# Kernel optimization log

Hardware: AMD Instinct MI355X
Metric: run time of the kernel (lower is better)

The kernel has to match this reference:

```python
import jax, jax.numpy as jnp
import numpy as np

N_NODES = 100000
N_EDGES = 1600000
N_LABEL = 200000
HID = 128
OUT = 5


def setup_inputs() -> dict:
    key = jax.random.key(0)
    k1, k2, k3, k4, k5 = jax.random.split(key, 5)
    x = jax.random.normal(k1, (N_NODES, HID), dtype=jnp.float32)
    edge_index = jax.random.randint(k2, (2, N_EDGES), 0, N_NODES, dtype=jnp.int64)
    edge_label_index = jax.random.randint(k3, (2, N_LABEL), 0, N_NODES, dtype=jnp.int64)
    W_gcn = jax.random.normal(k4, (HID, HID), dtype=jnp.float32) / np.sqrt(HID)
    b_gcn = jnp.zeros((HID,), dtype=jnp.float32)
    W_lin = jax.random.normal(k5, (2 * HID, OUT), dtype=jnp.float32) / np.sqrt(2 * HID)
    b_lin = jnp.zeros((OUT,), dtype=jnp.float32)
    return {"x": x, "edge_index": edge_index, "edge_label_index": edge_label_index,
            "W_gcn": W_gcn, "b_gcn": b_gcn, "W_lin": W_lin, "b_lin": b_lin}


def _gcn_conv(x, edge_index, W, b):
    # PyG GCNConv defaults: add self-loops, symmetric normalization,
    # linear transform first, then scatter-add of norm * x[src] into dst.
    n = x.shape[0]
    loop = jnp.arange(n, dtype=edge_index.dtype)
    src = jnp.concatenate([edge_index[0], loop])  # [E+N]
    dst = jnp.concatenate([edge_index[1], loop])  # [E+N]
    xw = x @ W  # [N, H]
    ones = jnp.ones(src.shape[0], dtype=x.dtype)
    deg = jax.ops.segment_sum(ones, dst, num_segments=n)  # in-degree incl self-loop
    dinv = jnp.where(deg > 0, jax.lax.rsqrt(deg), 0.0)
    norm = dinv[src] * dinv[dst]  # [E+N]
    msgs = xw[src] * norm[:, None]  # [E+N, H] gather + scale
    out = jax.ops.segment_sum(msgs, dst, num_segments=n)  # scatter-add
    return out + b


def reference(x, edge_index, edge_label_index, W_gcn, b_gcn, W_lin, b_lin):
    h = _gcn_conv(x, edge_index, W_gcn, b_gcn)  # [N, H]
    drug_emb = h[edge_label_index[0]]  # [E_label, H]
    prot_emb = h[edge_label_index[1]]  # [E_label, H]
    edge_emb = jnp.concatenate([drug_emb, prot_emb], axis=1)  # [E_label, 2H]
    return edge_emb @ W_lin + b_lin  # [E_label, OUT]
```

## Files before the change

### kernel.cpp

```cpp
#include <hip/hip_runtime.h>

#define N_NODES 100000
#define N_EDGES 1600000
#define N_LABEL 200000
#define HID 128
#define OUT 5

#define NBUCK 391
#define EPB   4096
#define NBLK_E 391
#define PREC_BLKS 9
#define BLD_K 20


__global__ __launch_bounds__(256) void k_hist(const int* __restrict__ ei,
                                              int* __restrict__ hist,
                                              const float* __restrict__ Wg,
                                              const float* __restrict__ bg,
                                              const float* __restrict__ Wl,
                                              float* __restrict__ G,
                                              int* __restrict__ total) {
    const int t = threadIdx.x, b = blockIdx.x;
    if (b >= NBLK_E) {
        if (b == NBLK_E && t == 0) *total = 0;
        int o = (b - NBLK_E) * 256 + t;
        if (o < 129 * 16) {
            int r = o >> 4, jj = o & 15;
            float acc = 0.f;
            if (jj < 2 * OUT) {
                const int half = (jj >= OUT);
                const int j = half ? jj - OUT : jj;
                for (int c = 0; c < HID; ++c) {
                    float w2 = Wl[(half * HID + c) * OUT + j];
                    float a = (r < HID) ? Wg[r * HID + c] : bg[c];
                    acc += a * w2;
                }
            }
            G[o] = acc;
        }
        return;
    }
    __shared__ int h[NBUCK];
    for (int i = t; i < NBUCK; i += 256) h[i] = 0;
    __syncthreads();
    const int e0 = b * EPB;
#pragma unroll
    for (int i = 0; i < 16; ++i) {
        int e = e0 + i * 256 + t;
        if (e < N_EDGES) atomicAdd(&h[ei[N_EDGES + e] >> 8], 1);
    }
    __syncthreads();
    for (int i = t; i < NBUCK; i += 256) hist[i * NBLK_E + b] = h[i];
}

__global__ __launch_bounds__(256) void k_scanb(int* __restrict__ hist,
                                               int* __restrict__ btot,
                                               int* __restrict__ bbase,
                                               int* __restrict__ total) {
    __shared__ int part[256];
    const int b = blockIdx.x, t = threadIdx.x;
    int* row = hist + b * NBLK_E;
    const int lo = t * 2, hi = min(lo + 2, NBLK_E);
    int v[2]; int s = 0;
    for (int i = lo; i < hi; ++i) { v[i - lo] = row[i]; s += v[i - lo]; }
    part[t] = s;
    __syncthreads();
#pragma unroll
    for (int off = 1; off < 256; off <<= 1) {
        int a = (t >= off) ? part[t - off] : 0;
        __syncthreads();
        part[t] += a;
        __syncthreads();
    }
    int run = part[t] - s;
    for (int i = lo; i < hi; ++i) { int x = v[i - lo]; row[i] = run; run += x; }
    if (t == 255) {
        int tot = part[255];
        btot[b] = tot;
        bbase[b] = atomicAdd(total, tot);
    }
}

__global__ __launch_bounds__(256) void k_part(const int* __restrict__ ei,
                                              const int* __restrict__ hist,
                                              const int* __restrict__ bbase,
                                              unsigned* __restrict__ bedge) {
    __shared__ int cur[NBUCK];
    const int t = threadIdx.x, b = blockIdx.x;
    for (int i = t; i < NBUCK; i += 256) cur[i] = bbase[i] + hist[i * NBLK_E + b];
    __syncthreads();
    const int e0 = b * EPB;
#pragma unroll
    for (int i = 0; i < 16; ++i) {
        int e = e0 + i * 256 + t;
        if (e < N_EDGES) {
            int dst = ei[N_EDGES + e];
            unsigned src = (unsigned)ei[e];
            int pos = atomicAdd(&cur[dst >> 8], 1);
            bedge[pos] = src | ((unsigned)(dst & 255) << 20);
        }
    }
}

__global__ __launch_bounds__(256) void k_build(const unsigned* __restrict__ bedge,
                                               const int* __restrict__ bbase,
                                               const int* __restrict__ btot,
                                               int* __restrict__ csr,
                                               int2* __restrict__ seg,
                                               float* __restrict__ dinv) {
    __shared__ int cnt[256];
    __shared__ int nb[256];
    __shared__ int cursor[256];
    const int b = blockIdx.x, t = threadIdx.x;
    const int base = bbase[b];
    const int size = btot[b];
    cnt[t] = 0;
    __syncthreads();

    unsigned ev[BLD_K];
#pragma unroll
    for (int c = 0; c < BLD_K; ++c) {
        int i = t + c * 256;
        unsigned v = 0xFFFFFFFFu;
        if (i < size) {
            v = bedge[base + i];
            atomicAdd(&cnt[v >> 20], 1);
        }
        ev[c] = v;
    }
    for (int i = t + BLD_K * 256; i < size; i += 256)
        atomicAdd(&cnt[bedge[base + i] >> 20], 1);
    __syncthreads();

    const int c = cnt[t];
    nb[t] = c;
    __syncthreads();
#pragma unroll
    for (int off = 1; off < 256; off <<= 1) {
        int a = (t >= off) ? nb[t - off] : 0;
        __syncthreads();
        nb[t] += a;
        __syncthreads();
    }
    const int myBase = nb[t] - c;
    cursor[t] = myBase;
    __syncthreads();

#pragma unroll
    for (int cc = 0; cc < BLD_K; ++cc) {
        unsigned v = ev[cc];
        if (v != 0xFFFFFFFFu) {
            int pos = atomicAdd(&cursor[v >> 20], 1);
            csr[base + pos] = (int)(v & 0xFFFFFu);
        }
    }
    for (int i = t + BLD_K * 256; i < size; i += 256) {
        unsigned v = bedge[base + i];
        int pos = atomicAdd(&cursor[v >> 20], 1);
        csr[base + pos] = (int)(v & 0xFFFFFu);
    }

    const int n = b * 256 + t;
    if (n < N_NODES) {
        seg[n] = make_int2(base + myBase, c);
        dinv[n] = rsqrtf((float)(c + 1));
    }
}

__global__ __launch_bounds__(256) void k_t(const float* __restrict__ x,
                                           const float* __restrict__ G,
                                           const float* __restrict__ dinv,
                                           float* __restrict__ t) {
    __shared__ float Gs[HID * 11];
    const int tid = threadIdx.x;
    for (int o = tid; o < HID * 10; o += 256) {
        int k = o / 10, j = o - k * 10;
        Gs[k * 11 + j] = G[k * 16 + j];
    }
    __syncthreads();

    int gid = blockIdx.x * 256 + tid;
    int n = gid >> 4;
    int i = gid & 15;

    const float4* x4 = (const float4*)x;
    float4 a0 = x4[(size_t)n * 32 + i];
    float4 a1 = x4[(size_t)n * 32 + 16 + i];
    float xv[8] = {a0.x, a0.y, a0.z, a0.w, a1.x, a1.y, a1.z, a1.w};

    float p[10];
#pragma unroll
    for (int j = 0; j < 10; ++j) p[j] = 0.f;
#pragma unroll
    for (int m = 0; m < 8; ++m) {
        const int k = (m < 4) ? (4 * i + m) : (64 + 4 * i + (m - 4));
        const float* g = &Gs[k * 11];
#pragma unroll
        for (int j = 0; j < 10; ++j) p[j] += xv[m] * g[j];
    }
#pragma unroll
    for (int off = 1; off < 16; off <<= 1) {
#pragma unroll
        for (int j = 0; j < 10; ++j) p[j] += __shfl_xor(p[j], off);
    }
    float val = (i == 0) ? p[0] : (i == 1) ? p[1] : (i == 2) ? p[2] : (i == 3) ? p[3] :
                (i == 4) ? p[4] : (i == 5) ? p[5] : (i == 6) ? p[6] : (i == 7) ? p[7] :
                (i == 8) ? p[8] : (i == 9) ? p[9] : 0.f;
    t[(size_t)n * 16 + i] = dinv[n] * val;
}

__global__ __launch_bounds__(256) void k_pullt(const float* __restrict__ t,
                                               const int2* __restrict__ seg,
                                               const int* __restrict__ csr,
                                               const float* __restrict__ dinv,
                                               const float* __restrict__ G,
                                               float* __restrict__ proj) {
    int gid = blockIdx.x * 256 + threadIdx.x;
    int n = gid >> 4;
    int i = gid & 15;
    const int gbase = threadIdx.x & 48;

    float acc = t[(size_t)n * 16 + i];
    const int2 sg = seg[n];
    const int beg = sg.x, deg = sg.y;

    for (int base = 0; base < deg; base += 16) {
        const int cnt = min(16, deg - base);
        int idx = (i < cnt) ? csr[beg + base + i] : 0;
        int j = 0;
        for (; j + 8 <= cnt; j += 8) {
            int s0 = __shfl(idx, gbase + j);
            int s1 = __shfl(idx, gbase + j + 1);
            int s2 = __shfl(idx, gbase + j + 2);
            int s3 = __shfl(idx, gbase + j + 3);
            int s4 = __shfl(idx, gbase + j + 4);
            int s5 = __shfl(idx, gbase + j + 5);
            int s6 = __shfl(idx, gbase + j + 6);
            int s7 = __shfl(idx, gbase + j + 7);
            float v0 = t[(size_t)s0 * 16 + i];
            float v1 = t[(size_t)s1 * 16 + i];
            float v2 = t[(size_t)s2 * 16 + i];
            float v3 = t[(size_t)s3 * 16 + i];
            float v4 = t[(size_t)s4 * 16 + i];
            float v5 = t[(size_t)s5 * 16 + i];
            float v6 = t[(size_t)s6 * 16 + i];
            float v7 = t[(size_t)s7 * 16 + i];
            acc += v0; acc += v1; acc += v2; acc += v3;
            acc += v4; acc += v5; acc += v6; acc += v7;
        }
        for (; j + 4 <= cnt; j += 4) {
            int s0 = __shfl(idx, gbase + j);
            int s1 = __shfl(idx, gbase + j + 1);
            int s2 = __shfl(idx, gbase + j + 2);
            int s3 = __shfl(idx, gbase + j + 3);
            float v0 = t[(size_t)s0 * 16 + i];
            float v1 = t[(size_t)s1 * 16 + i];
            float v2 = t[(size_t)s2 * 16 + i];
            float v3 = t[(size_t)s3 * 16 + i];
            acc += v0; acc += v1; acc += v2; acc += v3;
        }
        for (; j < cnt; ++j) {
            int s = __shfl(idx, gbase + j);
            acc += t[(size_t)s * 16 + i];
        }
    }
    proj[(size_t)n * 16 + i] = dinv[n] * acc + G[HID * 16 + i];
}

__global__ __launch_bounds__(256) void k_link2(const int* __restrict__ eli,
                                               const float* __restrict__ proj,
                                               const float* __restrict__ bl,
                                               float* __restrict__ out) {
    int idx = blockIdx.x * 256 + threadIdx.x;
    if (idx >= N_LABEL * OUT) return;
    int l = idx / OUT;
    int o = idx - l * OUT;
    int d = eli[l];
    int p = eli[N_LABEL + l];
    out[idx] = proj[d * 16 + o] + proj[p * 16 + OUT + o] + bl[o];
}

extern "C" void kernel_launch(void* const* d_in, const int* in_sizes, int n_in,
                              void* d_out, int out_size, void* d_ws, size_t ws_size,
                              hipStream_t stream) {
    const float* x     = (const float*)d_in[0];
    const int*   ei    = (const int*)d_in[1];
    const int*   eli   = (const int*)d_in[2];
    const float* W_gcn = (const float*)d_in[3];
    const float* b_gcn = (const float*)d_in[4];
    const float* W_lin = (const float*)d_in[5];
    const float* b_lin = (const float*)d_in[6];
    float* out = (float*)d_out;

    float* t         = (float*)d_ws;
    float* proj      = t + (size_t)N_NODES * 16;
    float* G         = proj + (size_t)N_NODES * 16;
    float* dinv      = G + 129 * 16;
    unsigned* bedge  = (unsigned*)(dinv + N_NODES);
    int*   csr       = (int*)(bedge + N_EDGES);
    int2*  seg       = (int2*)(csr + N_EDGES);
    int*   hist      = (int*)(seg + N_NODES);
    int*   btot      = hist + NBUCK * NBLK_E;
    int*   bbase     = btot + NBUCK;
    int*   total     = bbase + NBUCK;

    k_hist<<<NBLK_E + PREC_BLKS, 256, 0, stream>>>(ei, hist, W_gcn, b_gcn, W_lin, G, total);
    k_scanb<<<NBUCK, 256, 0, stream>>>(hist, btot, bbase, total);
    k_part<<<NBLK_E, 256, 0, stream>>>(ei, hist, bbase, bedge);
    k_build<<<NBUCK, 256, 0, stream>>>(bedge, bbase, btot, csr, seg, dinv);
    k_t<<<N_NODES * 16 / 256, 256, 0, stream>>>(x, G, dinv, t);
    k_pullt<<<N_NODES * 16 / 256, 256, 0, stream>>>(t, seg, csr, dinv, G, proj);
    k_link2<<<(N_LABEL * OUT + 255) / 256, 256, 0, stream>>>(eli, proj, b_lin, out);
}
```

Before: 108.4 us.

## Fuse CSR build stages into one cooperative kernel with grid syncs

Merges the histogram, bucket scan, partition and per-bucket CSR build kernels into a single cooperative launch that separates stages with grid.sync(). Destination indices are kept in LDS between the histogram and partition phases, so the partition phase does not reload them from global memory. This removes three kernel launch boundaries and one global read of the destination array. In exchange it pays for grid-wide barriers, depends on all 391 blocks being co-resident, and the larger LDS footprint may lower occupancy.

After: 270.9 us. +150.0%, slower.

```diff
diff --git a/kernel.cpp b/kernel.cpp
--- a/kernel.cpp
+++ b/kernel.cpp
@@ -1,4 +1,7 @@
 #include <hip/hip_runtime.h>
+#include <hip/hip_cooperative_groups.h>
+
+namespace cg = cooperative_groups;
 
 #define N_NODES 100000
 #define N_EDGES 1600000
@@ -9,21 +12,34 @@
 #define NBUCK 391
 #define EPB   4096
 #define NBLK_E 391
-#define PREC_BLKS 9
 #define BLD_K 20
 
 
-__global__ __launch_bounds__(256) void k_hist(const int* __restrict__ ei,
-                                              int* __restrict__ hist,
-                                              const float* __restrict__ Wg,
-                                              const float* __restrict__ bg,
-                                              const float* __restrict__ Wl,
-                                              float* __restrict__ G,
-                                              int* __restrict__ total) {
-    const int t = threadIdx.x, b = blockIdx.x;
-    if (b >= NBLK_E) {
-        if (b == NBLK_E && t == 0) *total = 0;
-        int o = (b - NBLK_E) * 256 + t;
+__global__ __launch_bounds__(256) void k_csr(const int* __restrict__ ei,
+                                             int* __restrict__ hist,
+                                             int* __restrict__ btot,
+                                             int* __restrict__ bbase,
+                                             int* __restrict__ total,
+                                             unsigned* __restrict__ bedge,
+                                             int* __restrict__ csr,
+                                             int2* __restrict__ seg,
+                                             float* __restrict__ dinv,
+                                             const float* __restrict__ Wg,
+                                             const float* __restrict__ bg,
+                                             const float* __restrict__ Wl,
+                                             float* __restrict__ G) {
+    cg::grid_group grid = cg::this_grid();
+    __shared__ int h[NBUCK];
+    __shared__ int dstl[EPB];
+    __shared__ int part[256];
+    __shared__ int cnt[256];
+    __shared__ int nb[256];
+    __shared__ int cursor[256];
+    const int b = blockIdx.x, t = threadIdx.x;
+
+    {
+        int o = b * 256 + t;
+        if (o == 0) *total = 0;
         if (o < 129 * 16) {
             int r = o >> 4, jj = o & 15;
             float acc = 0.f;
@@ -38,132 +54,118 @@
             }
             G[o] = acc;
         }
-        return;
-    }
-    __shared__ int h[NBUCK];
+    }
     for (int i = t; i < NBUCK; i += 256) h[i] = 0;
     __syncthreads();
     const int e0 = b * EPB;
 #pragma unroll
     for (int i = 0; i < 16; ++i) {
         int e = e0 + i * 256 + t;
-        if (e < N_EDGES) atomicAdd(&h[ei[N_EDGES + e] >> 8], 1);
+        if (e < N_EDGES) {
+            int d = ei[N_EDGES + e];
+            dstl[i * 256 + t] = d;
+            atomicAdd(&h[d >> 8], 1);
+        }
     }
     __syncthreads();
     for (int i = t; i < NBUCK; i += 256) hist[i * NBLK_E + b] = h[i];
-}
-
-__global__ __launch_bounds__(256) void k_scanb(int* __restrict__ hist,
-                                               int* __restrict__ btot,
-                                               int* __restrict__ bbase,
-                                               int* __restrict__ total) {
-    __shared__ int part[256];
-    const int b = blockIdx.x, t = threadIdx.x;
-    int* row = hist + b * NBLK_E;
-    const int lo = t * 2, hi = min(lo + 2, NBLK_E);
-    int v[2]; int s = 0;
-    for (int i = lo; i < hi; ++i) { v[i - lo] = row[i]; s += v[i - lo]; }
-    part[t] = s;
+
+    grid.sync();
+
+    {
+        int* row = hist + b * NBLK_E;
+        const int lo = t * 2, hi = min(lo + 2, NBLK_E);
+        int v[2]; int s = 0;
+        for (int i = lo; i < hi; ++i) { v[i - lo] = row[i]; s += v[i - lo]; }
+        part[t] = s;
+        __syncthreads();
+#pragma unroll
+        for (int off = 1; off < 256; off <<= 1) {
+            int a = (t >= off) ? part[t - off] : 0;
+            __syncthreads();
+            part[t] += a;
+            __syncthreads();
+        }
+        int run = part[t] - s;
+        for (int i = lo; i < hi; ++i) { int x = v[i - lo]; row[i] = run; run += x; }
+        if (t == 255) {
+            int tot = part[255];
+            btot[b] = tot;
+            bbase[b] = atomicAdd(total, tot);
+        }
+    }
+
+    grid.sync();
+
+    for (int i = t; i < NBUCK; i += 256) h[i] = bbase[i] + hist[i * NBLK_E + b];
     __syncthreads();
-#pragma unroll
-    for (int off = 1; off < 256; off <<= 1) {
-        int a = (t >= off) ? part[t - off] : 0;
-        __syncthreads();
-        part[t] += a;
-        __syncthreads();
-    }
-    int run = part[t] - s;
-    for (int i = lo; i < hi; ++i) { int x = v[i - lo]; row[i] = run; run += x; }
-    if (t == 255) {
-        int tot = part[255];
-        btot[b] = tot;
-        bbase[b] = atomicAdd(total, tot);
-    }
-}
-
-__global__ __launch_bounds__(256) void k_part(const int* __restrict__ ei,
-                                              const int* __restrict__ hist,
-                                              const int* __restrict__ bbase,
-                                              unsigned* __restrict__ bedge) {
-    __shared__ int cur[NBUCK];
-    const int t = threadIdx.x, b = blockIdx.x;
-    for (int i = t; i < NBUCK; i += 256) cur[i] = bbase[i] + hist[i * NBLK_E + b];
-    __syncthreads();
-    const int e0 = b * EPB;
 #pragma unroll
     for (int i = 0; i < 16; ++i) {
         int e = e0 + i * 256 + t;
         if (e < N_EDGES) {
-            int dst = ei[N_EDGES + e];
+            int d = dstl[i * 256 + t];
             unsigned src = (unsigned)ei[e];
-            int pos = atomicAdd(&cur[dst >> 8], 1);
-            bedge[pos] = src | ((unsigned)(dst & 255) << 20);
-        }
-    }
-}
-
-__global__ __launch_bounds__(256) void k_build(const unsigned* __restrict__ bedge,
-                                               const int* __restrict__ bbase,
-                                               const int* __restrict__ btot,
-                                               int* __restrict__ csr,
-                                               int2* __restrict__ seg,
-                                               float* __restrict__ dinv) {
-    __shared__ int cnt[256];
-    __shared__ int nb[256];
-    __shared__ int cursor[256];
-    const int b = blockIdx.x, t = threadIdx.x;
-    const int base = bbase[b];
-    const int size = btot[b];
-    cnt[t] = 0;
-    __syncthreads();
-
-    unsigned ev[BLD_K];
-#pragma unroll
-    for (int c = 0; c < BLD_K; ++c) {
-        int i = t + c * 256;
-        unsigned v = 0xFFFFFFFFu;
-        if (i < size) {
-            v = bedge[base + i];
-            atomicAdd(&cnt[v >> 20], 1);
-        }
-        ev[c] = v;
-    }
-    for (int i = t + BLD_K * 256; i < size; i += 256)
-        atomicAdd(&cnt[bedge[base + i] >> 20], 1);
-    __syncthreads();
-
-    const int c = cnt[t];
-    nb[t] = c;
-    __syncthreads();
-#pragma unroll
-    for (int off = 1; off < 256; off <<= 1) {
-        int a = (t >= off) ? nb[t - off] : 0;
-        __syncthreads();
-        nb[t] += a;
-        __syncthreads();
-    }
-    const int myBase = nb[t] - c;
-    cursor[t] = myBase;
-    __syncthreads();
-
-#pragma unroll
-    for (int cc = 0; cc < BLD_K; ++cc) {
-        unsigned v = ev[cc];
-        if (v != 0xFFFFFFFFu) {
+            int pos = atomicAdd(&h[d >> 8], 1);
+            bedge[pos] = src | ((unsigned)(d & 255) << 20);
+        }
+    }
+
+    grid.sync();
+
+    {
+        const int base = bbase[b];
+        const int size = btot[b];
+        cnt[t] = 0;
+        __syncthreads();
+
+        unsigned ev[BLD_K];
+#pragma unroll
+        for (int c = 0; c < BLD_K; ++c) {
+            int i = t + c * 256;
+            unsigned v = 0xFFFFFFFFu;
+            if (i < size) {
+                v = bedge[base + i];
+                atomicAdd(&cnt[v >> 20], 1);
+            }
+            ev[c] = v;
+        }
+        for (int i = t + BLD_K * 256; i < size; i += 256)
+            atomicAdd(&cnt[bedge[base + i] >> 20], 1);
+        __syncthreads();
+
+        const int c = cnt[t];
+        nb[t] = c;
+        __syncthreads();
+#pragma unroll
+        for (int off = 1; off < 256; off <<= 1) {
+            int a = (t >= off) ? nb[t - off] : 0;
+            __syncthreads();
+            nb[t] += a;
+            __syncthreads();
+        }
+        const int myBase = nb[t] - c;
+        cursor[t] = myBase;
+        __syncthreads();
+
+#pragma unroll
+        for (int cc = 0; cc < BLD_K; ++cc) {
+            unsigned v = ev[cc];
+            if (v != 0xFFFFFFFFu) {
+                int pos = atomicAdd(&cursor[v >> 20], 1);
+                csr[base + pos] = (int)(v & 0xFFFFFu);
+            }
+        }
+        for (int i = t + BLD_K * 256; i < size; i += 256) {
+            unsigned v = bedge[base + i];
             int pos = atomicAdd(&cursor[v >> 20], 1);
             csr[base + pos] = (int)(v & 0xFFFFFu);
         }
-    }
-    for (int i = t + BLD_K * 256; i < size; i += 256) {
-        unsigned v = bedge[base + i];
-        int pos = atomicAdd(&cursor[v >> 20], 1);
-        csr[base + pos] = (int)(v & 0xFFFFFu);
-    }
-
-    const int n = b * 256 + t;
-    if (n < N_NODES) {
-        seg[n] = make_int2(base + myBase, c);
-        dinv[n] = rsqrtf((float)(c + 1));
+
+        const int n = b * 256 + t;
+        if (n < N_NODES) {
+            seg[n] = make_int2(base + myBase, c);
+            dinv[n] = rsqrtf((float)(c + 1));
+        }
     }
 }
 
@@ -304,10 +306,13 @@
     int*   bbase     = btot + NBUCK;
     int*   total     = bbase + NBUCK;
 
-    k_hist<<<NBLK_E + PREC_BLKS, 256, 0, stream>>>(ei, hist, W_gcn, b_gcn, W_lin, G, total);
-    k_scanb<<<NBUCK, 256, 0, stream>>>(hist, btot, bbase, total);
-    k_part<<<NBLK_E, 256, 0, stream>>>(ei, hist, bbase, bedge);
-    k_build<<<NBUCK, 256, 0, stream>>>(bedge, bbase, btot, csr, seg, dinv);
+    {
+        void* args[] = {(void*)&ei, (void*)&hist, (void*)&btot, (void*)&bbase,
+                        (void*)&total, (void*)&bedge, (void*)&csr, (void*)&seg,
+                        (void*)&dinv, (void*)&W_gcn, (void*)&b_gcn, (void*)&W_lin,
+                        (void*)&G};
+        hipLaunchCooperativeKernel((void*)k_csr, dim3(NBLK_E), dim3(256), args, 0, stream);
+    }
     k_t<<<N_NODES * 16 / 256, 256, 0, stream>>>(x, G, dinv, t);
     k_pullt<<<N_NODES * 16 / 256, 256, 0, stream>>>(t, seg, csr, dinv, G, proj);
     k_link2<<<(N_LABEL * OUT + 255) / 256, 256, 0, stream>>>(eli, proj, b_lin, out);
```
